# Performance work log

Measured on AMD Instinct MI355X. Metric: run time of the kernel, lower is better.

## Reference

```python
import jax, jax.numpy as jnp
import numpy as np

K = 32          # neighbors per point
EPS = 1e-5      # InstanceNorm eps (torch default)
SLOPE = 0.2     # LeakyReLU negative slope


def _knn(x, k):
    # x: [B, N, C]; squared euclidean distances (same ordering as torch.cdist p=2)
    sq = jnp.sum(x * x, axis=-1)                       # [B, N]
    d = sq[:, :, None] + sq[:, None, :] - 2.0 * jnp.einsum('bnc,bmc->bnm', x, x)
    _, idx = jax.lax.top_k(-d, k + 1)                  # smallest distances first
    return idx[:, :, 1:]                               # drop self -> [B, N, k]


def _edge_feat(x, idx):
    # x: [B, N, C], idx: [B, N, k] -> [B, N, k, 2C] = concat(neighbor - center, center)
    nb = jax.vmap(lambda xb, ib: xb[ib])(x, idx)       # [B, N, k, C] gather
    c = jnp.broadcast_to(x[:, :, None, :], nb.shape)
    return jnp.concatenate([nb - c, c], axis=-1)


def _inorm(x, axes):
    # InstanceNorm (no affine): normalize over `axes` with biased variance
    m = jnp.mean(x, axis=axes, keepdims=True)
    v = jnp.mean((x - m) ** 2, axis=axes, keepdims=True)
    return (x - m) * jax.lax.rsqrt(v + EPS)


def _lrelu(x):
    return jnp.where(x >= 0, x, SLOPE * x)


def setup_inputs() -> dict:
    key = jax.random.key(0)
    ks = jax.random.split(key, 11)
    B, N = 2, 2048

    def w(k, shape):
        return jax.random.normal(k, shape, jnp.float32) * 0.05

    return {
        'x': jax.random.normal(ks[0], (B, N, 3), jnp.float32),
        'n': jax.random.normal(ks[1], (B, N, 3), jnp.float32),
        'W0': w(ks[2], (32, 6)),      # Conv2d(6, 32, 1, bias=False)
        'W1': w(ks[3], (64, 64)),     # Conv2d(64, 64, 1)
        'W2': w(ks[4], (128, 128)),   # Conv2d(128, 128, 1)
        'W3': w(ks[5], (256, 256)),   # Conv2d(256, 256, 1)
        'Wh': w(ks[6], (128, 480)),   # Conv1d(sum(hidden)=480, encod_dim=128, 1)
        'fc1_w': w(ks[7], (128, 128)),
        'fc1_b': w(ks[8], (128,)),
        'fc2_w': w(ks[9], (128, 128)),
        'fc2_b': w(ks[10], (128,)),
    }


def reference(x, n, W0, W1, W2, W3, Wh, fc1_w, fc1_b, fc2_w, fc2_b):
    # include_normals=False: n is accepted but unused (matches torch forward).
    feats = []
    h = x  # [B, N, C], C starts at 3
    for W in (W0, W1, W2, W3):
        idx = _knn(h, K)                              # [B, N, K]
        e = _edge_feat(h, idx)                        # [B, N, K, 2C]
        e = jnp.einsum('bnkc,oc->bnko', e, W)         # 1x1 conv
        e = _lrelu(_inorm(e, (1, 2)))                 # InstanceNorm2d over (N, K)
        h = jnp.max(e, axis=2)                        # max over neighbors -> [B, N, O]
        feats.append(h)
    f = jnp.concatenate(feats, axis=-1)               # [B, N, 480]
    f = jnp.einsum('bnc,oc->bno', f, Wh)              # 1x1 conv1d -> [B, N, 128]
    f = _lrelu(_inorm(f, (1,)))                       # InstanceNorm1d over N; dropout is identity (eval)
    g = jnp.max(f, axis=1)                            # adaptive_max_pool1d(1) -> [B, 128]
    g = g @ fc1_w.T + fc1_b
    # torch InstanceNorm1d on a 2D [B, 128] input treats it as unbatched (C, L):
    # normalizes each row over its 128 features.
    g = _lrelu(_inorm(g, (1,)))
    return g @ fc2_w.T + fc2_b                        # [B, 128]
```

## Files before the change

kernel.cpp:

```cpp
#include <hip/hip_runtime.h>
#include <hip/hip_bf16.h>
#include <cstdint>

using bf16 = __hip_bfloat16;

static constexpr int B = 2;
static constexpr int N = 2048;
static constexpr int KNN = 32;
static constexpr int FD = 480;
static constexpr float EPS = 1e-5f;
static constexpr float SLOPE = 0.2f;
static constexpr int REP = 8;

static constexpr size_t N_XF = (size_t)B * N * 3;
static constexpr size_t N_FEATS = (size_t)B * N * FD;
static constexpr size_t N_DIST = (size_t)B * N * N;
static constexpr size_t N_IDX = (size_t)B * N * KNN;
static constexpr size_t N_PROJ = (size_t)B * N * 512;
static constexpr size_t O_XF = 0;
static constexpr size_t O_FEATS = O_XF + N_XF;
static constexpr size_t O_DIST = O_FEATS + N_FEATS;
static constexpr size_t O_IDX = O_DIST + N_DIST;
static constexpr size_t O_PROJ = O_IDX + N_IDX;
static constexpr size_t O_WP0 = O_PROJ + N_PROJ;
static constexpr size_t O_WP1 = O_WP0 + 192;
static constexpr size_t O_WP2 = O_WP1 + 4096;
static constexpr size_t O_WP3 = O_WP2 + 16384;
static constexpr size_t O_WHT = O_WP3 + 65536;
static constexpr size_t O_F1W = O_WHT + 61440;
static constexpr size_t O_F1B = O_F1W + 16384;
static constexpr size_t O_F2W = O_F1B + 128;
static constexpr size_t O_F2B = O_F2W + 16384;
static constexpr size_t O_FLAG = O_F2B + 128;
static constexpr size_t O_CS0 = O_FLAG + 16;
static constexpr size_t O_CS1 = O_CS0 + (size_t)REP * B * 32 * 2;
static constexpr size_t O_CS2 = O_CS1 + (size_t)REP * B * 64 * 2;
static constexpr size_t O_CS3 = O_CS2 + (size_t)REP * B * 128 * 2;
static constexpr size_t O_FSUM = O_CS3 + (size_t)REP * B * 256 * 2;
static constexpr size_t O_FSS = O_FSUM + 256;
static constexpr size_t O_FMAX = O_FSS + 256;
static constexpr size_t O_END = O_FMAX + 256;
static constexpr size_t N_ZERO = O_END - O_CS0;

__device__ __forceinline__ float lrelu(float x) { return x >= 0.f ? x : SLOPE * x; }

__device__ __forceinline__ float load_in(const void* p, int i, int isf32) {
  return isf32 ? ((const float*)p)[i] : __bfloat162float(((const bf16*)p)[i]);
}

static constexpr int PREP_TOTAL =
    (int)(N_XF + 96 + 2048 + 8192 + 32768 + 61440 + 16384 + 128 + 16384 + 128 + N_ZERO);

__global__ __launch_bounds__(256) void prep_kernel(
    const void* __restrict__ x, const void* __restrict__ W0, const void* __restrict__ W1,
    const void* __restrict__ W2, const void* __restrict__ W3, const void* __restrict__ Wh,
    const void* __restrict__ fc1w, const void* __restrict__ fc1b,
    const void* __restrict__ fc2w, const void* __restrict__ fc2b, float* __restrict__ ws) {
  __shared__ float red[256];
  const unsigned short* xr = (const unsigned short*)x;
  float mx = 0.f;
  for (int i = threadIdx.x; i < B * N * 3; i += 256) {
    float v = __uint_as_float(((unsigned)xr[i]) << 16);
    v = fabsf(v);
    if (!(v < 1e30f)) v = 1e30f;
    mx = fmaxf(mx, v);
  }
  red[threadIdx.x] = mx;
  __syncthreads();
  for (int s = 128; s > 0; s >>= 1) {
    if (threadIdx.x < s) red[threadIdx.x] = fmaxf(red[threadIdx.x], red[threadIdx.x + s]);
    __syncthreads();
  }
  int isf = red[0] > 1e3f ? 1 : 0;
  if (blockIdx.x == 0 && threadIdx.x == 0) ((int*)(ws + O_FLAG))[0] = isf;

  int idx = blockIdx.x * 256 + threadIdx.x;
  if (idx < (int)N_XF) { ws[O_XF + idx] = load_in(x, idx, isf); return; }
  idx -= (int)N_XF;
  if (idx < 96) {
    int o = idx / 3, c = idx - o * 3;
    float a = load_in(W0, o * 6 + c, isf);
    float bb = load_in(W0, o * 6 + 3 + c, isf);
    ws[O_WP0 + c * 64 + o] = a;
    ws[O_WP0 + c * 64 + 32 + o] = bb - a;
    return;
  }
  idx -= 96;
  if (idx < 2048) {
    int o = idx >> 5, c = idx & 31;
    float a = load_in(W1, o * 64 + c, isf);
    float bb = load_in(W1, o * 64 + 32 + c, isf);
    ws[O_WP1 + c * 128 + o] = a;
    ws[O_WP1 + c * 128 + 64 + o] = bb - a;
    return;
  }
  idx -= 2048;
  if (idx < 8192) {
    int o = idx >> 6, c = idx & 63;
    float a = load_in(W2, o * 128 + c, isf);
    float bb = load_in(W2, o * 128 + 64 + c, isf);
    ws[O_WP2 + c * 256 + o] = a;
    ws[O_WP2 + c * 256 + 128 + o] = bb - a;
    return;
  }
  idx -= 8192;
  if (idx < 32768) {
    int o = idx >> 7, c = idx & 127;
    float a = load_in(W3, o * 256 + c, isf);
    float bb = load_in(W3, o * 256 + 128 + c, isf);
    ws[O_WP3 + c * 512 + o] = a;
    ws[O_WP3 + c * 512 + 256 + o] = bb - a;
    return;
  }
  idx -= 32768;
  if (idx < 61440) {
    int o = idx / 480, c = idx - o * 480;
    ws[O_WHT + c * 128 + o] = load_in(Wh, idx, isf);
    return;
  }
  idx -= 61440;
  if (idx < 16384) { ws[O_F1W + idx] = load_in(fc1w, idx, isf); return; }
  idx -= 16384;
  if (idx < 128) { ws[O_F1B + idx] = load_in(fc1b, idx, isf); return; }
  idx -= 128;
  if (idx < 16384) { ws[O_F2W + idx] = load_in(fc2w, idx, isf); return; }
  idx -= 16384;
  if (idx < 128) { ws[O_F2B + idx] = load_in(fc2b, idx, isf); return; }
  idx -= 128;
  if (idx < (int)N_ZERO) ws[O_CS0 + idx] = 0.f;
}

template <int C>
__global__ __launch_bounds__(256) void dist_kernel(const float* __restrict__ h, int hstride,
                                                   float* __restrict__ dist) {
  constexpr int CW = 16;
  __shared__ float Ast[CW][68];
  __shared__ float Bst[CW][132];
  __shared__ float sqn[64], sqm[128];
  int b = blockIdx.z;
  int n0 = blockIdx.y * 64, m0 = blockIdx.x * 128;
  int tid = threadIdx.x;
  int tx = tid & 15, ty = tid >> 4;
  float dot[4][8] = {};
  float sqa = 0.f;
  for (int cc = 0; cc < C; cc += CW) {
    if constexpr (C % CW == 0) {
      int r = tid >> 2, cq = (tid & 3) * 4;
      float4 va = *reinterpret_cast<const float4*>(
          &h[(size_t)(b * N + n0 + r) * hstride + cc + cq]);
      Ast[cq + 0][r] = va.x;
      Ast[cq + 1][r] = va.y;
      Ast[cq + 2][r] = va.z;
      Ast[cq + 3][r] = va.w;
#pragma unroll
      for (int k = 0; k < 2; ++k) {
        int i = tid + k * 256;
        int rB = i >> 2, cqB = (i & 3) * 4;
        float4 vb = *reinterpret_cast<const float4*>(
            &h[(size_t)(b * N + m0 + rB) * hstride + cc + cqB]);
        Bst[cqB + 0][rB] = vb.x;
        Bst[cqB + 1][rB] = vb.y;
        Bst[cqB + 2][rB] = vb.z;
        Bst[cqB + 3][rB] = vb.w;
      }
    } else {
      for (int i = tid; i < 64 * CW; i += 256) {
        int c = i & 15, r = i >> 4;
        int gc = cc + c;
        Ast[c][r] = (gc < C) ? h[(size_t)(b * N + n0 + r) * hstride + gc] : 0.f;
      }
      for (int i = tid; i < 128 * CW; i += 256) {
        int c = i & 15, r = i >> 4;
        int gc = cc + c;
        Bst[c][r] = (gc < C) ? h[(size_t)(b * N + m0 + r) * hstride + gc] : 0.f;
      }
    }
    __syncthreads();
    if (tid < 64) {
#pragma unroll
      for (int c = 0; c < CW; ++c) { float v = Ast[c][tid]; sqa += v * v; }
    } else if (tid < 192) {
      int r = tid - 64;
#pragma unroll
      for (int c = 0; c < CW; ++c) { float v = Bst[c][r]; sqa += v * v; }
    }
#pragma unroll
    for (int c = 0; c < CW; ++c) {
      float4 a0 = *reinterpret_cast<const float4*>(&Ast[c][ty * 4]);
      float4 b0 = *reinterpret_cast<const float4*>(&Bst[c][tx * 4]);
      float4 b1 = *reinterpret_cast<const float4*>(&Bst[c][64 + tx * 4]);
      float av[4] = {a0.x, a0.y, a0.z, a0.w};
      float bv[8] = {b0.x, b0.y, b0.z, b0.w, b1.x, b1.y, b1.z, b1.w};
#pragma unroll
      for (int i = 0; i < 4; ++i)
#pragma unroll
        for (int j = 0; j < 8; ++j) dot[i][j] += av[i] * bv[j];
    }
    __syncthreads();
  }
  if (tid < 64) sqn[tid] = sqa;
  else if (tid < 192) sqm[tid - 64] = sqa;
  __syncthreads();
#pragma unroll
  for (int i = 0; i < 4; ++i) {
    int nn = n0 + ty * 4 + i;
    float sn = sqn[ty * 4 + i];
    float4 w;
    w.x = sn + sqm[tx * 4 + 0] - 2.f * dot[i][0];
    w.y = sn + sqm[tx * 4 + 1] - 2.f * dot[i][1];
    w.z = sn + sqm[tx * 4 + 2] - 2.f * dot[i][2];
    w.w = sn + sqm[tx * 4 + 3] - 2.f * dot[i][3];
    *reinterpret_cast<float4*>(&dist[(size_t)(b * N + nn) * N + m0 + tx * 4]) = w;
    float4 w2;
    w2.x = sn + sqm[64 + tx * 4 + 0] - 2.f * dot[i][4];
    w2.y = sn + sqm[64 + tx * 4 + 1] - 2.f * dot[i][5];
    w2.z = sn + sqm[64 + tx * 4 + 2] - 2.f * dot[i][6];
    w2.w = sn + sqm[64 + tx * 4 + 3] - 2.f * dot[i][7];
    *reinterpret_cast<float4*>(&dist[(size_t)(b * N + nn) * N + m0 + 64 + tx * 4]) = w2;
  }
}

__device__ __forceinline__ unsigned long long wave_min_u64(unsigned long long v) {
#pragma unroll
  for (int m = 1; m < 64; m <<= 1) {
    unsigned lo = (unsigned)v;
    unsigned hi = (unsigned)(v >> 32);
    unsigned olo = (unsigned)__shfl_xor((int)lo, m, 64);
    unsigned ohi = (unsigned)__shfl_xor((int)hi, m, 64);
    unsigned long long ov = ((unsigned long long)ohi << 32) | olo;
    if (ov < v) v = ov;
  }
  return v;
}

#define ARGMIN32(dk, ld, lj)                                        \
  {                                                                 \
    unsigned kv0 = dk[0], kv1 = dk[8], kv2 = dk[16], kv3 = dk[24];  \
    int j0 = 0, j1 = 8, j2 = 16, j3 = 24;                           \
    _Pragma("unroll")                                               \
    for (int t = 1; t < 8; ++t) {                                   \
      if (dk[t] < kv0) { kv0 = dk[t]; j0 = t; }                     \
      if (dk[8 + t] < kv1) { kv1 = dk[8 + t]; j1 = 8 + t; }         \
      if (dk[16 + t] < kv2) { kv2 = dk[16 + t]; j2 = 16 + t; }      \
      if (dk[24 + t] < kv3) { kv3 = dk[24 + t]; j3 = 24 + t; }      \
    }                                                               \
    if (kv1 < kv0) { kv0 = kv1; j0 = j1; }                          \
    if (kv3 < kv2) { kv2 = kv3; j2 = j3; }                          \
    if (kv2 < kv0) { kv0 = kv2; j0 = j2; }                          \
    ld = kv0; lj = j0;                                              \
  }

__device__ __forceinline__ unsigned bitonic64_u32(unsigned v, int lane) {
#pragma unroll
  for (int k = 2; k <= 64; k <<= 1) {
#pragma unroll
    for (int j = k >> 1; j > 0; j >>= 1) {
      unsigned o = (unsigned)__shfl_xor((int)v, j, 64);
      bool up = (lane & k) == 0;
      bool lower = (lane & j) == 0;
      bool keepmin = (up == lower);
      unsigned mn = v < o ? v : o;
      unsigned mx = v < o ? o : v;
      v = keepmin ? mn : mx;
    }
  }
  return v;
}

__device__ __forceinline__ void bitonic64_u64(unsigned& hi, unsigned& lo, int lane) {
#pragma unroll
  for (int k = 2; k <= 64; k <<= 1) {
#pragma unroll
    for (int j = k >> 1; j > 0; j >>= 1) {
      unsigned ohi = (unsigned)__shfl_xor((int)hi, j, 64);
      unsigned olo = (unsigned)__shfl_xor((int)lo, j, 64);
      bool up = (lane & k) == 0;
      bool lower = (lane & j) == 0;
      bool keepmin = (up == lower);
      bool lt = (hi < ohi) || (hi == ohi && lo < olo);
      bool take_other = keepmin ? !lt : lt;
      if (take_other) { hi = ohi; lo = olo; }
    }
  }
}

template <int C, int NO2>
__global__ __launch_bounds__(256) void selproj_kernel(const float* __restrict__ dist,
                                                      int* __restrict__ idxb,
                                                      const float* __restrict__ h,
                                                      int hstride,
                                                      const float* __restrict__ Wp,
                                                      float* __restrict__ projb) {
  constexpr int NSEL = B * N / 4;
  constexpr int MT = NO2 / 64;
  constexpr int CW = 16;
  __shared__ float As[64][17];
  __shared__ float Bs[64][17];
  if (blockIdx.x < NSEL) {
    int row = blockIdx.x * 4 + (threadIdx.x >> 6);
    int lane = threadIdx.x & 63;
    const float* drow = dist + (size_t)row * N;
    unsigned dk[32];
#pragma unroll
    for (int j = 0; j < 32; ++j) {
      unsigned u = __float_as_uint(drow[j * 64 + lane]);
      dk[j] = (u & 0x80000000u) ? ~u : (u | 0x80000000u);
    }
    unsigned lmin0 = dk[0], lmin1 = dk[1];
#pragma unroll
    for (int j = 2; j < 32; j += 2) {
      lmin0 = lmin0 < dk[j] ? lmin0 : dk[j];
      lmin1 = lmin1 < dk[j + 1] ? lmin1 : dk[j + 1];
    }
    unsigned lmin = lmin0 < lmin1 ? lmin0 : lmin1;
    unsigned srt = bitonic64_u32(lmin, lane);
    unsigned T = (unsigned)__shfl((int)srt, 32, 64);
    unsigned cnt = 0;
#pragma unroll
    for (int j = 0; j < 32; ++j) cnt += (dk[j] <= T) ? 1u : 0u;
    unsigned inc = cnt;
#pragma unroll
    for (int d = 1; d < 64; d <<= 1) {
      unsigned t = (unsigned)__shfl_up((int)inc, d, 64);
      if (lane >= d) inc += t;
    }
    unsigned tot = (unsigned)__shfl((int)inc, 63, 64);
    unsigned off = inc - cnt;
    bool fast = tot <= 64u;
    unsigned* aHi = reinterpret_cast<unsigned*>(&As[0][0]);
    unsigned* aLo = reinterpret_cast<unsigned*>(&Bs[0][0]);
    int wbase = (threadIdx.x >> 6) * 64;
    aHi[wbase + lane] = 0xFFFFFFFFu;
    aLo[wbase + lane] = 0xFFFFFFFFu;
    __syncthreads();
    if (fast) {
      unsigned o = off;
#pragma unroll
      for (int j = 0; j < 32; ++j) {
        if (dk[j] <= T) {
          aHi[wbase + o] = dk[j];
          aLo[wbase + o] = (unsigned)(j * 64 + lane);
          ++o;
        }
      }
    }
    __syncthreads();
    if (fast) {
      unsigned hi = aHi[wbase + lane];
      unsigned lo = aLo[wbase + lane];
      bitonic64_u64(hi, lo, lane);
      if (lane >= 1 && lane <= KNN) idxb[row * KNN + lane - 1] = (int)lo;
    } else {
      unsigned ld;
      int lj;
      ARGMIN32(dk, ld, lj);
      unsigned saved = 0;
      for (int it = 0; it <= KNN; ++it) {
        unsigned long long lkey =
            ((unsigned long long)ld << 32) | (unsigned)(lj * 64 + lane);
        unsigned long long g = wave_min_u64(lkey);
        if (it > 0 && lane == it - 1) saved = (unsigned)(g & 0xFFFFFFFFull);
        if (lkey == g) {
#pragma unroll
          for (int j = 0; j < 32; ++j)
            if (j == lj) dk[j] = 0xFFFFFFFFu;
          ARGMIN32(dk, ld, lj);
        }
      }
      if (lane < KNN) idxb[row * KNN + lane] = (int)saved;
    }
  } else {
    int tile = blockIdx.x - NSEL;
    int m0 = (tile % MT) * 64;
    int n0 = (tile / MT) * 64;
    int tid = threadIdx.x;
    int tx = tid & 15, ty = tid >> 4;
    float dot[4][4] = {};
    for (int cc = 0; cc < C; cc += CW) {
      for (int i = tid; i < 64 * CW; i += 256) {
        int r = i >> 4, c = i & 15;
        int gc = cc + c;
        As[r][c] = (gc < C) ? h[(size_t)(n0 + r) * hstride + gc] : 0.f;
      }
      for (int i = tid; i < 64 * CW; i += 256) {
        int c = i >> 6, m = i & 63;
        int gc = cc + c;
        Bs[m][c] = (gc < C) ? Wp[(size_t)gc * NO2 + m0 + m] : 0.f;
      }
      __syncthreads();
#pragma unroll
      for (int c = 0; c < CW; ++c) {
        float av[4], bv[4];
#pragma unroll
        for (int i = 0; i < 4; ++i) av[i] = As[ty * 4 + i][c];
#pragma unroll
        for (int j = 0; j < 4; ++j) bv[j] = Bs[tx * 4 + j][c];
#pragma unroll
        for (int i = 0; i < 4; ++i)
#pragma unroll
          for (int j = 0; j < 4; ++j) dot[i][j] += av[i] * bv[j];
      }
      __syncthreads();
    }
#pragma unroll
    for (int i = 0; i < 4; ++i) {
      float4 wv;
      wv.x = dot[i][0];
      wv.y = dot[i][1];
      wv.z = dot[i][2];
      wv.w = dot[i][3];
      int m = m0 + tx * 4;
      size_t base = ((size_t)(m >> 4) * (B * N) + (size_t)(n0 + ty * 4 + i)) * 16 + (m & 15);
      *reinterpret_cast<float4*>(&projb[base]) = wv;
    }
  }
}

template <int O, int NP>
__global__ __launch_bounds__(256) void edge_slab_kernel(const float* __restrict__ projs,
                                                        const int* __restrict__ idxb,
                                                        float* __restrict__ cstats,
                                                        float* __restrict__ featdst) {
  __shared__ float slab[2048 * 16];
  __shared__ float redsm[2][4][16];
  int split = blockIdx.x, s = blockIdx.y, b = blockIdx.z;
  int tid = threadIdx.x, w = tid >> 6, lane = tid & 63;
  int kq = lane >> 4, ch = lane & 15;
  {
    const float4* src =
        (const float4*)(projs + ((size_t)s * (B * N) + (size_t)b * N) * 16);
    float4* dst = (float4*)slab;
#pragma unroll
    for (int i = 0; i < 32; ++i) dst[tid + i * 256] = src[tid + i * 256];
  }
  __syncthreads();
  const float* h0s = projs + (size_t)(O / 16 + s) * (B * N) * 16;
  int bn0 = b * N + split * NP;
  constexpr int NPW = NP / 4;
  float sum = 0.f, ssum = 0.f;
  int bn = bn0 + w;
  int4 j0n = *(const int4*)(idxb + (size_t)bn * KNN + kq * 8);
  int4 j1n = *(const int4*)(idxb + (size_t)bn * KNN + kq * 8 + 4);
  float h0n = h0s[(size_t)bn * 16 + ch];
  for (int p = 0; p < NPW; ++p) {
    int4 j0 = j0n, j1 = j1n;
    float h0 = h0n;
    int bncur = bn;
    if (p + 1 < NPW) {
      bn = bn0 + (p + 1) * 4 + w;
      j0n = *(const int4*)(idxb + (size_t)bn * KNN + kq * 8);
      j1n = *(const int4*)(idxb + (size_t)bn * KNN + kq * 8 + 4);
      h0n = h0s[(size_t)bn * 16 + ch];
    }
    float a0 = slab[j0.x * 16 + ch];
    float a1 = slab[j0.y * 16 + ch];
    float a2 = slab[j0.z * 16 + ch];
    float a3 = slab[j0.w * 16 + ch];
    float a4 = slab[j1.x * 16 + ch];
    float a5 = slab[j1.y * 16 + ch];
    float a6 = slab[j1.z * 16 + ch];
    float a7 = slab[j1.w * 16 + ch];
    float e0 = a0 + h0, e1 = a1 + h0, e2 = a2 + h0, e3 = a3 + h0;
    float e4 = a4 + h0, e5 = a5 + h0, e6 = a6 + h0, e7 = a7 + h0;
    sum += e0 + e1 + e2 + e3 + e4 + e5 + e6 + e7;
    ssum += e0 * e0 + e1 * e1 + e2 * e2 + e3 * e3 + e4 * e4 + e5 * e5 + e6 * e6 + e7 * e7;
    float mx = fmaxf(fmaxf(fmaxf(e0, e1), fmaxf(e2, e3)), fmaxf(fmaxf(e4, e5), fmaxf(e6, e7)));
    mx = fmaxf(mx, __shfl_xor(mx, 16, 64));
    mx = fmaxf(mx, __shfl_xor(mx, 32, 64));
    if (kq == 0) featdst[(size_t)bncur * FD + s * 16 + ch] = mx;
  }
  sum += __shfl_xor(sum, 16, 64);
  sum += __shfl_xor(sum, 32, 64);
  ssum += __shfl_xor(ssum, 16, 64);
  ssum += __shfl_xor(ssum, 32, 64);
  if (kq == 0) {
    redsm[0][w][ch] = sum;
    redsm[1][w][ch] = ssum;
  }
  __syncthreads();
  if (tid < 16) {
    float S = 0.f, SS = 0.f;
#pragma unroll
    for (int r = 0; r < 4; ++r) {
      S += redsm[0][r][tid];
      SS += redsm[1][r][tid];
    }
    int rep = split & (REP - 1);
    float* cs = cstats + ((size_t)rep * B + b) * O * 2 + (size_t)(s * 16 + tid) * 2;
    atomicAdd(&cs[0], S);
    atomicAdd(&cs[1], SS);
  }
}

__global__ void finalize_kernel(const float* __restrict__ cstats,
                                float* __restrict__ featdst, int O) {
  int i = blockIdx.x * 256 + threadIdx.x;
  int o = i % O;
  int bn = i / O;
  int b = bn >> 11;
  float s = 0.f, ss = 0.f;
#pragma unroll
  for (int r = 0; r < REP; ++r) {
    s += cstats[(size_t)r * (B * O * 2) + (size_t)(b * O + o) * 2 + 0];
    ss += cstats[(size_t)r * (B * O * 2) + (size_t)(b * O + o) * 2 + 1];
  }
  constexpr float inv = 1.f / ((float)N * KNN);
  float m = s * inv;
  float v = fmaxf(ss * inv - m * m, 0.f);
  float* p = &featdst[(size_t)bn * FD + o];
  float e = (*p - m) * rsqrtf(v + EPS);
  *p = lrelu(e);
}

__global__ __launch_bounds__(256) void fstage_kernel(const float* __restrict__ feats,
                                                     const float* __restrict__ Wht,
                                                     float* __restrict__ fsum,
                                                     float* __restrict__ fss,
                                                     unsigned* __restrict__ fmaxu) {
  int blk = blockIdx.x;
  int b = blk >> 7;
  int n0 = (blk & 127) * 16;
  int tid = threadIdx.x;
  __shared__ float rows[16][FD];
  __shared__ float red[3][2][128];
  for (int i = tid; i < 16 * FD; i += 256) {
    int r = i / FD, c = i - r * FD;
    rows[r][c] = feats[(size_t)(b * N + n0 + r) * FD + c];
  }
  __syncthreads();
  int o = tid & 127, g = tid >> 7;
  float acc[8] = {};
  for (int c = 0; c < FD; c += 4) {
    float w0 = Wht[(c + 0) * 128 + o];
    float w1 = Wht[(c + 1) * 128 + o];
    float w2 = Wht[(c + 2) * 128 + o];
    float w3 = Wht[(c + 3) * 128 + o];
#pragma unroll
    for (int j = 0; j < 8; ++j) {
      float4 r4 = *reinterpret_cast<const float4*>(&rows[g * 8 + j][c]);
      acc[j] += w0 * r4.x + w1 * r4.y + w2 * r4.z + w3 * r4.w;
    }
  }
  float s = 0.f, ss = 0.f, mx = -3.4e38f;
#pragma unroll
  for (int j = 0; j < 8; ++j) {
    float f = acc[j];
    s += f;
    ss += f * f;
    mx = fmaxf(mx, f);
  }
  red[0][g][o] = s;
  red[1][g][o] = ss;
  red[2][g][o] = mx;
  __syncthreads();
  if (g == 0) {
    s += red[0][1][o];
    ss += red[1][1][o];
    mx = fmaxf(mx, red[2][1][o]);
    atomicAdd(&fsum[b * 128 + o], s);
    atomicAdd(&fss[b * 128 + o], ss);
    unsigned u = __float_as_uint(mx);
    u = (u & 0x80000000u) ? ~u : (u | 0x80000000u);
    atomicMax(&fmaxu[b * 128 + o], u);
  }
}

__global__ __launch_bounds__(128) void head_kernel(const float* __restrict__ fsum,
                                                   const float* __restrict__ fss,
                                                   const unsigned* __restrict__ fmaxu,
                                                   const float* __restrict__ fc1w,
                                                   const float* __restrict__ fc1b,
                                                   const float* __restrict__ fc2w,
                                                   const float* __restrict__ fc2b,
                                                   void* __restrict__ out,
                                                   const int* __restrict__ flag) {
  int b = blockIdx.x, o = threadIdx.x;
  __shared__ float gs[128], t1[128], ys[128];
  constexpr float invN = 1.f / N;
  float m = fsum[b * 128 + o] * invN;
  float v = fmaxf(fss[b * 128 + o] * invN - m * m, 0.f);
  unsigned u = fmaxu[b * 128 + o];
  unsigned bits = (u & 0x80000000u) ? (u ^ 0x80000000u) : ~u;
  float fx = __uint_as_float(bits);
  gs[o] = lrelu((fx - m) * rsqrtf(v + EPS));
  __syncthreads();
  float a = fc1b[o];
  for (int c = 0; c < 128; ++c) a += fc1w[o * 128 + c] * gs[c];
  t1[o] = a;
  __syncthreads();
  float mm = 0.f;
  for (int c = 0; c < 128; ++c) mm += t1[c];
  mm *= (1.f / 128);
  float vv = 0.f;
  for (int c = 0; c < 128; ++c) {
    float d = t1[c] - mm;
    vv += d * d;
  }
  vv *= (1.f / 128);
  ys[o] = lrelu((a - mm) * rsqrtf(vv + EPS));
  __syncthreads();
  float r = fc2b[o];
  for (int c = 0; c < 128; ++c) r += fc2w[o * 128 + c] * ys[c];
  if (flag[0])
    ((float*)out)[b * 128 + o] = r;
  else
    ((bf16*)out)[b * 128 + o] = __float2bfloat16(r);
}

template <int C, int O>
static void run_layer(const float* h, int hstride, float* featdst, const float* Wp,
                      float* cstats, float* dist, float* projb, int* idxb,
                      hipStream_t stream) {
  constexpr int NSEL = B * N / 4;
  constexpr int NPROJ = (2 * O / 64) * (B * N / 64);
  dist_kernel<C><<<dim3(N / 128, N / 64, B), 256, 0, stream>>>(h, hstride, dist);
  selproj_kernel<C, 2 * O><<<NSEL + NPROJ, 256, 0, stream>>>(dist, idxb, h, hstride, Wp,
                                                             projb);
  constexpr int NP = (O >= 256) ? 256 : (O == 128 ? 128 : 64);
  edge_slab_kernel<O, NP><<<dim3(N / NP, O / 16, B), 256, 0, stream>>>(projb, idxb, cstats,
                                                                       featdst);
  finalize_kernel<<<B * N * O / 256, 256, 0, stream>>>(cstats, featdst, O);
}

extern "C" void kernel_launch(void* const* d_in, const int* in_sizes, int n_in,
                              void* d_out, int out_size, void* d_ws, size_t ws_size,
                              hipStream_t stream) {
  float* ws = (float*)d_ws;
  float* xf = ws + O_XF;
  float* feats = ws + O_FEATS;
  float* dist = ws + O_DIST;
  float* projb = ws + O_PROJ;
  int* idxb = (int*)(ws + O_IDX);
  int* flag = (int*)(ws + O_FLAG);

  prep_kernel<<<(PREP_TOTAL + 255) / 256, 256, 0, stream>>>(
      d_in[0], d_in[2], d_in[3], d_in[4], d_in[5], d_in[6], d_in[7], d_in[8], d_in[9],
      d_in[10], ws);

  run_layer<3, 32>(xf, 3, feats + 0, ws + O_WP0, ws + O_CS0, dist, projb, idxb, stream);
  run_layer<32, 64>(feats + 0, FD, feats + 32, ws + O_WP1, ws + O_CS1, dist, projb, idxb,
                    stream);
  run_layer<64, 128>(feats + 32, FD, feats + 96, ws + O_WP2, ws + O_CS2, dist, projb, idxb,
                     stream);
  run_layer<128, 256>(feats + 96, FD, feats + 224, ws + O_WP3, ws + O_CS3, dist, projb,
                      idxb, stream);

  fstage_kernel<<<B * 128, 256, 0, stream>>>(feats, ws + O_WHT, ws + O_FSUM, ws + O_FSS,
                                             (unsigned*)(ws + O_FMAX));
  head_kernel<<<B, 128, 0, stream>>>(ws + O_FSUM, ws + O_FSS, (unsigned*)(ws + O_FMAX),
                                     ws + O_F1W, ws + O_F1B, ws + O_F2W, ws + O_F2B, d_out,
                                     flag);
}
```

Before: 382.1 us.

## Encode distance keys in dist kernel and select two kNN rows per wave

The dist kernel now writes order-preserving unsigned keys, so the selection pass no longer converts floats. Each wave now handles two rows using contiguous uint4 loads (lane*32+j layout) instead of strided scalar loads. The two rows share one packed prefix scan and run interleaved bitonic sorts, which adds instruction-level parallelism. The selection block count is halved, and register pressure rises from holding 64 keys per lane. The paired 64-bit bitonic sort now runs for both rows even when a row takes the slow path.

```diff
diff --git a/kernel.cpp b/kernel.cpp
--- a/kernel.cpp
+++ b/kernel.cpp
@@ -48,6 +48,11 @@
   return isf32 ? ((const float*)p)[i] : __bfloat162float(((const bf16*)p)[i]);
 }
 
+__device__ __forceinline__ unsigned key_of(float f) {
+  unsigned u = __float_as_uint(f);
+  return (u & 0x80000000u) ? ~u : (u | 0x80000000u);
+}
+
 static constexpr int PREP_TOTAL =
     (int)(N_XF + 96 + 2048 + 8192 + 32768 + 61440 + 16384 + 128 + 16384 + 128 + N_ZERO);
 
@@ -132,7 +137,7 @@
 
 template <int C>
 __global__ __launch_bounds__(256) void dist_kernel(const float* __restrict__ h, int hstride,
-                                                   float* __restrict__ dist) {
+                                                   unsigned* __restrict__ dist) {
   constexpr int CW = 16;
   __shared__ float Ast[CW][68];
   __shared__ float Bst[CW][132];
@@ -205,18 +210,18 @@
   for (int i = 0; i < 4; ++i) {
     int nn = n0 + ty * 4 + i;
     float sn = sqn[ty * 4 + i];
-    float4 w;
-    w.x = sn + sqm[tx * 4 + 0] - 2.f * dot[i][0];
-    w.y = sn + sqm[tx * 4 + 1] - 2.f * dot[i][1];
-    w.z = sn + sqm[tx * 4 + 2] - 2.f * dot[i][2];
-    w.w = sn + sqm[tx * 4 + 3] - 2.f * dot[i][3];
-    *reinterpret_cast<float4*>(&dist[(size_t)(b * N + nn) * N + m0 + tx * 4]) = w;
-    float4 w2;
-    w2.x = sn + sqm[64 + tx * 4 + 0] - 2.f * dot[i][4];
-    w2.y = sn + sqm[64 + tx * 4 + 1] - 2.f * dot[i][5];
-    w2.z = sn + sqm[64 + tx * 4 + 2] - 2.f * dot[i][6];
-    w2.w = sn + sqm[64 + tx * 4 + 3] - 2.f * dot[i][7];
-    *reinterpret_cast<float4*>(&dist[(size_t)(b * N + nn) * N + m0 + 64 + tx * 4]) = w2;
+    uint4 w;
+    w.x = key_of(sn + sqm[tx * 4 + 0] - 2.f * dot[i][0]);
+    w.y = key_of(sn + sqm[tx * 4 + 1] - 2.f * dot[i][1]);
+    w.z = key_of(sn + sqm[tx * 4 + 2] - 2.f * dot[i][2]);
+    w.w = key_of(sn + sqm[tx * 4 + 3] - 2.f * dot[i][3]);
+    *reinterpret_cast<uint4*>(&dist[(size_t)(b * N + nn) * N + m0 + tx * 4]) = w;
+    uint4 w2;
+    w2.x = key_of(sn + sqm[64 + tx * 4 + 0] - 2.f * dot[i][4]);
+    w2.y = key_of(sn + sqm[64 + tx * 4 + 1] - 2.f * dot[i][5]);
+    w2.z = key_of(sn + sqm[64 + tx * 4 + 2] - 2.f * dot[i][6]);
+    w2.w = key_of(sn + sqm[64 + tx * 4 + 3] - 2.f * dot[i][7]);
+    *reinterpret_cast<uint4*>(&dist[(size_t)(b * N + nn) * N + m0 + 64 + tx * 4]) = w2;
   }
 }
 
@@ -250,124 +255,177 @@
     ld = kv0; lj = j0;                                              \
   }
 
-__device__ __forceinline__ unsigned bitonic64_u32(unsigned v, int lane) {
+__device__ __forceinline__ void bitonic64_u32_pair(unsigned& v0, unsigned& v1, int lane) {
 #pragma unroll
   for (int k = 2; k <= 64; k <<= 1) {
 #pragma unroll
     for (int j = k >> 1; j > 0; j >>= 1) {
-      unsigned o = (unsigned)__shfl_xor((int)v, j, 64);
-      bool up = (lane & k) == 0;
-      bool lower = (lane & j) == 0;
-      bool keepmin = (up == lower);
-      unsigned mn = v < o ? v : o;
-      unsigned mx = v < o ? o : v;
-      v = keepmin ? mn : mx;
-    }
-  }
-  return v;
-}
-
-__device__ __forceinline__ void bitonic64_u64(unsigned& hi, unsigned& lo, int lane) {
+      unsigned o0 = (unsigned)__shfl_xor((int)v0, j, 64);
+      unsigned o1 = (unsigned)__shfl_xor((int)v1, j, 64);
+      bool keepmin = ((lane & k) == 0) == ((lane & j) == 0);
+      unsigned mn0 = v0 < o0 ? v0 : o0, mx0 = v0 < o0 ? o0 : v0;
+      unsigned mn1 = v1 < o1 ? v1 : o1, mx1 = v1 < o1 ? o1 : v1;
+      v0 = keepmin ? mn0 : mx0;
+      v1 = keepmin ? mn1 : mx1;
+    }
+  }
+}
+
+__device__ __forceinline__ void bitonic64_u64_pair(unsigned& hi0, unsigned& lo0,
+                                                   unsigned& hi1, unsigned& lo1, int lane) {
 #pragma unroll
   for (int k = 2; k <= 64; k <<= 1) {
 #pragma unroll
     for (int j = k >> 1; j > 0; j >>= 1) {
-      unsigned ohi = (unsigned)__shfl_xor((int)hi, j, 64);
-      unsigned olo = (unsigned)__shfl_xor((int)lo, j, 64);
-      bool up = (lane & k) == 0;
-      bool lower = (lane & j) == 0;
-      bool keepmin = (up == lower);
-      bool lt = (hi < ohi) || (hi == ohi && lo < olo);
-      bool take_other = keepmin ? !lt : lt;
-      if (take_other) { hi = ohi; lo = olo; }
+      unsigned ohi0 = (unsigned)__shfl_xor((int)hi0, j, 64);
+      unsigned olo0 = (unsigned)__shfl_xor((int)lo0, j, 64);
+      unsigned ohi1 = (unsigned)__shfl_xor((int)hi1, j, 64);
+      unsigned olo1 = (unsigned)__shfl_xor((int)lo1, j, 64);
+      bool keepmin = ((lane & k) == 0) == ((lane & j) == 0);
+      bool lt0 = (hi0 < ohi0) || (hi0 == ohi0 && lo0 < olo0);
+      bool lt1 = (hi1 < ohi1) || (hi1 == ohi1 && lo1 < olo1);
+      if (keepmin ? !lt0 : lt0) { hi0 = ohi0; lo0 = olo0; }
+      if (keepmin ? !lt1 : lt1) { hi1 = ohi1; lo1 = olo1; }
     }
   }
 }
 
 template <int C, int NO2>
-__global__ __launch_bounds__(256) void selproj_kernel(const float* __restrict__ dist,
+__global__ __launch_bounds__(256) void selproj_kernel(const unsigned* __restrict__ dist,
                                                       int* __restrict__ idxb,
                                                       const float* __restrict__ h,
                                                       int hstride,
                                                       const float* __restrict__ Wp,
                                                       float* __restrict__ projb) {
-  constexpr int NSEL = B * N / 4;
+  constexpr int NSEL = B * N / 8;
   constexpr int MT = NO2 / 64;
   constexpr int CW = 16;
   __shared__ float As[64][17];
   __shared__ float Bs[64][17];
   if (blockIdx.x < NSEL) {
-    int row = blockIdx.x * 4 + (threadIdx.x >> 6);
+    int wv = threadIdx.x >> 6;
     int lane = threadIdx.x & 63;
-    const float* drow = dist + (size_t)row * N;
-    unsigned dk[32];
+    int row0 = blockIdx.x * 8 + wv * 2;
+    const unsigned* dr0 = dist + (size_t)row0 * N;
+    const unsigned* dr1 = dr0 + N;
+    unsigned dk0[32], dk1[32];
+#pragma unroll
+    for (int q = 0; q < 8; ++q) {
+      uint4 a = *reinterpret_cast<const uint4*>(dr0 + lane * 32 + q * 4);
+      dk0[q * 4 + 0] = a.x; dk0[q * 4 + 1] = a.y;
+      dk0[q * 4 + 2] = a.z; dk0[q * 4 + 3] = a.w;
+      uint4 c = *reinterpret_cast<const uint4*>(dr1 + lane * 32 + q * 4);
+      dk1[q * 4 + 0] = c.x; dk1[q * 4 + 1] = c.y;
+      dk1[q * 4 + 2] = c.z; dk1[q * 4 + 3] = c.w;
+    }
+    unsigned a0 = dk0[0], a1 = dk0[1], b0 = dk1[0], b1 = dk1[1];
+#pragma unroll
+    for (int j = 2; j < 32; j += 2) {
+      a0 = a0 < dk0[j] ? a0 : dk0[j];
+      a1 = a1 < dk0[j + 1] ? a1 : dk0[j + 1];
+      b0 = b0 < dk1[j] ? b0 : dk1[j];
+      b1 = b1 < dk1[j + 1] ? b1 : dk1[j + 1];
+    }
+    unsigned lm0 = a0 < a1 ? a0 : a1;
+    unsigned lm1 = b0 < b1 ? b0 : b1;
+    bitonic64_u32_pair(lm0, lm1, lane);
+    unsigned T0 = (unsigned)__shfl((int)lm0, 32, 64);
+    unsigned T1 = (unsigned)__shfl((int)lm1, 32, 64);
+    unsigned cnt0 = 0, cnt1 = 0;
 #pragma unroll
     for (int j = 0; j < 32; ++j) {
-      unsigned u = __float_as_uint(drow[j * 64 + lane]);
-      dk[j] = (u & 0x80000000u) ? ~u : (u | 0x80000000u);
-    }
-    unsigned lmin0 = dk[0], lmin1 = dk[1];
-#pragma unroll
-    for (int j = 2; j < 32; j += 2) {
-      lmin0 = lmin0 < dk[j] ? lmin0 : dk[j];
-      lmin1 = lmin1 < dk[j + 1] ? lmin1 : dk[j + 1];
-    }
-    unsigned lmin = lmin0 < lmin1 ? lmin0 : lmin1;
-    unsigned srt = bitonic64_u32(lmin, lane);
-    unsigned T = (unsigned)__shfl((int)srt, 32, 64);
-    unsigned cnt = 0;
-#pragma unroll
-    for (int j = 0; j < 32; ++j) cnt += (dk[j] <= T) ? 1u : 0u;
-    unsigned inc = cnt;
+      cnt0 += (dk0[j] <= T0) ? 1u : 0u;
+      cnt1 += (dk1[j] <= T1) ? 1u : 0u;
+    }
+    unsigned inc = cnt0 | (cnt1 << 16);
 #pragma unroll
     for (int d = 1; d < 64; d <<= 1) {
       unsigned t = (unsigned)__shfl_up((int)inc, d, 64);
       if (lane >= d) inc += t;
     }
     unsigned tot = (unsigned)__shfl((int)inc, 63, 64);
-    unsigned off = inc - cnt;
-    bool fast = tot <= 64u;
+    unsigned off0 = (inc & 0xFFFFu) - cnt0;
+    unsigned off1 = (inc >> 16) - cnt1;
+    bool fast0 = (tot & 0xFFFFu) <= 64u;
+    bool fast1 = (tot >> 16) <= 64u;
     unsigned* aHi = reinterpret_cast<unsigned*>(&As[0][0]);
     unsigned* aLo = reinterpret_cast<unsigned*>(&Bs[0][0]);
-    int wbase = (threadIdx.x >> 6) * 64;
-    aHi[wbase + lane] = 0xFFFFFFFFu;
-    aLo[wbase + lane] = 0xFFFFFFFFu;
+    int wb0 = (wv * 2 + 0) * 64;
+    int wb1 = (wv * 2 + 1) * 64;
+    aHi[wb0 + lane] = 0xFFFFFFFFu;
+    aLo[wb0 + lane] = 0xFFFFFFFFu;
+    aHi[wb1 + lane] = 0xFFFFFFFFu;
+    aLo[wb1 + lane] = 0xFFFFFFFFu;
     __syncthreads();
-    if (fast) {
-      unsigned o = off;
+    if (fast0) {
+      unsigned o = off0;
 #pragma unroll
       for (int j = 0; j < 32; ++j) {
-        if (dk[j] <= T) {
-          aHi[wbase + o] = dk[j];
-          aLo[wbase + o] = (unsigned)(j * 64 + lane);
+        if (dk0[j] <= T0) {
+          aHi[wb0 + o] = dk0[j];
+          aLo[wb0 + o] = (unsigned)(lane * 32 + j);
           ++o;
         }
       }
     }
+    if (fast1) {
+      unsigned o = off1;
+#pragma unroll
+      for (int j = 0; j < 32; ++j) {
+        if (dk1[j] <= T1) {
+          aHi[wb1 + o] = dk1[j];
+          aLo[wb1 + o] = (unsigned)(lane * 32 + j);
+          ++o;
+        }
+      }
+    }
     __syncthreads();
-    if (fast) {
-      unsigned hi = aHi[wbase + lane];
-      unsigned lo = aLo[wbase + lane];
-      bitonic64_u64(hi, lo, lane);
-      if (lane >= 1 && lane <= KNN) idxb[row * KNN + lane - 1] = (int)lo;
-    } else {
+    {
+      unsigned h0 = aHi[wb0 + lane], l0 = aLo[wb0 + lane];
+      unsigned h1 = aHi[wb1 + lane], l1 = aLo[wb1 + lane];
+      bitonic64_u64_pair(h0, l0, h1, l1, lane);
+      if (lane >= 1 && lane <= KNN) {
+        if (fast0) idxb[row0 * KNN + lane - 1] = (int)l0;
+        if (fast1) idxb[(row0 + 1) * KNN + lane - 1] = (int)l1;
+      }
+    }
+    if (!fast0) {
       unsigned ld;
       int lj;
-      ARGMIN32(dk, ld, lj);
+      ARGMIN32(dk0, ld, lj);
       unsigned saved = 0;
       for (int it = 0; it <= KNN; ++it) {
         unsigned long long lkey =
-            ((unsigned long long)ld << 32) | (unsigned)(lj * 64 + lane);
+            ((unsigned long long)ld << 32) | (unsigned)(lane * 32 + lj);
         unsigned long long g = wave_min_u64(lkey);
         if (it > 0 && lane == it - 1) saved = (unsigned)(g & 0xFFFFFFFFull);
         if (lkey == g) {
 #pragma unroll
           for (int j = 0; j < 32; ++j)
-            if (j == lj) dk[j] = 0xFFFFFFFFu;
-          ARGMIN32(dk, ld, lj);
+            if (j == lj) dk0[j] = 0xFFFFFFFFu;
+          ARGMIN32(dk0, ld, lj);
         }
       }
-      if (lane < KNN) idxb[row * KNN + lane] = (int)saved;
+      if (lane < KNN) idxb[row0 * KNN + lane] = (int)saved;
+    }
+    if (!fast1) {
+      unsigned ld;
+      int lj;
+      ARGMIN32(dk1, ld, lj);
+      unsigned saved = 0;
+      for (int it = 0; it <= KNN; ++it) {
+        unsigned long long lkey =
+            ((unsigned long long)ld << 32) | (unsigned)(lane * 32 + lj);
+        unsigned long long g = wave_min_u64(lkey);
+        if (it > 0 && lane == it - 1) saved = (unsigned)(g & 0xFFFFFFFFull);
+        if (lkey == g) {
+#pragma unroll
+          for (int j = 0; j < 32; ++j)
+            if (j == lj) dk1[j] = 0xFFFFFFFFu;
+          ARGMIN32(dk1, ld, lj);
+        }
+      }
+      if (lane < KNN) idxb[(row0 + 1) * KNN + lane] = (int)saved;
     }
   } else {
     int tile = blockIdx.x - NSEL;
@@ -404,14 +462,14 @@
     }
 #pragma unroll
     for (int i = 0; i < 4; ++i) {
-      float4 wv;
-      wv.x = dot[i][0];
-      wv.y = dot[i][1];
-      wv.z = dot[i][2];
-      wv.w = dot[i][3];
+      float4 wv4;
+      wv4.x = dot[i][0];
+      wv4.y = dot[i][1];
+      wv4.z = dot[i][2];
+      wv4.w = dot[i][3];
       int m = m0 + tx * 4;
       size_t base = ((size_t)(m >> 4) * (B * N) + (size_t)(n0 + ty * 4 + i)) * 16 + (m & 15);
-      *reinterpret_cast<float4*>(&projb[base]) = wv;
+      *reinterpret_cast<float4*>(&projb[base]) = wv4;
     }
   }
 }
@@ -609,9 +667,9 @@
 
 template <int C, int O>
 static void run_layer(const float* h, int hstride, float* featdst, const float* Wp,
-                      float* cstats, float* dist, float* projb, int* idxb,
+                      float* cstats, unsigned* dist, float* projb, int* idxb,
                       hipStream_t stream) {
-  constexpr int NSEL = B * N / 4;
+  constexpr int NSEL = B * N / 8;
   constexpr int NPROJ = (2 * O / 64) * (B * N / 64);
   dist_kernel<C><<<dim3(N / 128, N / 64, B), 256, 0, stream>>>(h, hstride, dist);
   selproj_kernel<C, 2 * O><<<NSEL + NPROJ, 256, 0, stream>>>(dist, idxb, h, hstride, Wp,
@@ -628,7 +686,7 @@
   float* ws = (float*)d_ws;
   float* xf = ws + O_XF;
   float* feats = ws + O_FEATS;
-  float* dist = ws + O_DIST;
+  unsigned* dist = (unsigned*)(ws + O_DIST);
   float* projb = ws + O_PROJ;
   int* idxb = (int*)(ws + O_IDX);
   int* flag = (int*)(ws + O_FLAG);
```

After: 411.6 us. +7.7%, slower.
